# Performance work log

Measured on AMD Instinct MI355X. Metric: run time of the kernel, lower is better.

The kernel has to match this reference:

```python
import jax, jax.numpy as jnp
import numpy as np
from jax import lax

H = 256        # hidden_size
T = 576        # history length (PERIOD*24)
F_T = 24       # future steps
M = 32         # m_features
B = 256        # batch
PERIOD = T // 24
E = 2 * H      # encoder output dim (bidirectional)
EPS = 1e-6     # torch PairwiseDistance eps


def setup_inputs() -> dict:
    key = jax.random.key(0)
    ks = jax.random.split(key, 16)
    rn = lambda k, sh, s=1.0: jax.random.normal(k, sh, jnp.float32) * s
    return {
        "input_encoded": rn(ks[0], (B, T, E)),
        "feature_history1": rn(ks[1], (B, T, M)),
        "y_history": rn(ks[2], (B, T, 1)),               # unused by forward (matches torch)
        "feature_future1": rn(ks[3], (B, F_T, M)),
        "hidden": rn(ks[4], (2, B, H), 0.1),
        "cell": rn(ks[5], (2, B, H), 0.1),
        # attn_layer: Linear(2H+M -> T), Tanh, Linear(T -> T)
        "attn_W1": rn(ks[6], (T, E + M), 0.05), "attn_b1": jnp.zeros((T,), jnp.float32),
        "attn_W2": rn(ks[7], (T, T), 0.05),     "attn_b2": jnp.zeros((T,), jnp.float32),
        # bidirectional 1-layer LSTM, stacked over direction d in {fwd, bwd}
        "W_ih": rn(ks[8], (2, 4 * H, E + M), 0.05),
        "W_hh": rn(ks[9], (2, 4 * H, H), 0.05),
        "b_ih": jnp.zeros((2, 4 * H), jnp.float32),
        "b_hh": jnp.zeros((2, 4 * H), jnp.float32),
        # fc_final: Linear(2H -> H), ReLU, Linear(H -> 1)
        "fcf_W1": rn(ks[10], (H, E), 0.05), "fcf_b1": jnp.zeros((H,), jnp.float32),
        "fcf_W2": rn(ks[11], (1, H), 0.05), "fcf_b2": jnp.zeros((1,), jnp.float32),
    }


def reference(input_encoded, feature_history1, y_history, feature_future1,
              hidden, cell, attn_W1, attn_b1, attn_W2, attn_b2,
              W_ih, W_hh, b_ih, b_hh, fcf_W1, fcf_b1, fcf_W2, fcf_b2):
    b = input_encoded.shape[0]
    # --- period-similarity weights alpha (computed once) ---
    fh = feature_history1.reshape(b, PERIOD, 24, M)                 # [B,period,24,M]
    # pairwise L2 distance between future [B,24,1,M] and history hours [B,24,period,M]
    diff = feature_future1[:, :, None, :] - fh.transpose(0, 2, 1, 3)  # [B,24,period,M]
    dist = jnp.sqrt(jnp.sum((diff + EPS) ** 2, axis=-1))            # [B,24,period]
    dp = 1.0 / jnp.sum(dist, axis=2)                                # rsqrt(.)**2 == 1/x; [B,24]
    alpha = jax.nn.softmax(dp, axis=1)                              # [B,24] (period==24)
    enc = input_encoded.reshape(b, PERIOD, 24, E)                   # [B,period,24,E]
    bias = (b_ih + b_hh)[:, None, :]                                # [2,1,4H]

    def step(carry, ff_t):                                          # ff_t: [B,M]
        h, c = carry                                                # each [2,B,H]
        x = jnp.concatenate([h[0], h[1], ff_t], axis=1)             # [B,2H+M]
        a = jnp.tanh(x @ attn_W1.T + attn_b1) @ attn_W2.T + attn_b2
        a = jax.nn.softmax(a, axis=1)                               # [B,T]
        w = a.reshape(b, PERIOD, 24)                                # [B,period,24]
        # context: sum attention-weighted encodings over each day, then alpha over periods
        ctx = jnp.einsum('bpk,bpke,bp->be', w, enc, alpha)          # [B,E]
        inp = jnp.concatenate([ctx, ff_t], axis=1)                  # [B,2H+M]
        gates = (jnp.einsum('bi,dgi->dbg', inp, W_ih)
                 + jnp.einsum('dbh,dgh->dbg', h, W_hh) + bias)      # [2,B,4H]
        i_g, f_g, g_g, o_g = jnp.split(gates, 4, axis=-1)           # torch gate order i,f,g,o
        c_new = jax.nn.sigmoid(f_g) * c + jax.nn.sigmoid(i_g) * jnp.tanh(g_g)
        h_new = jax.nn.sigmoid(o_g) * jnp.tanh(c_new)               # [2,B,H]
        hh = jnp.concatenate([h_new[0], h_new[1]], axis=1)          # [B,2H]
        y = jax.nn.relu(hh @ fcf_W1.T + fcf_b1) @ fcf_W2.T + fcf_b2  # [B,1]
        return (h_new, c_new), y

    _, ys = lax.scan(step, (hidden, cell), jnp.transpose(feature_future1, (1, 0, 2)))
    return jnp.transpose(ys, (1, 0, 2))                             # [B,f_T,1]
```

## Files before the change

kernel.cpp:

```cpp
#include <hip/hip_runtime.h>
#include <math.h>

#define B_ 256
#define T_ 576
#define FT_ 24
#define M_ 32
#define H_ 256
#define E_ 512
#define KX_ 544
#define G_ 1024
#define ND_ 2048
#define EPS_ 1e-6f

typedef __attribute__((ext_vector_type(8))) short bf8;
typedef __attribute__((ext_vector_type(4))) float f4;

__device__ __forceinline__ float bf2f(unsigned short s) {
    union { unsigned u; float f; } c; c.u = ((unsigned)s) << 16; return c.f;
}
__device__ __forceinline__ short f2bf(float f) {
    union { float f; unsigned u; } c; c.f = f;
    unsigned r = c.u + 0x7fffu + ((c.u >> 16) & 1u);
    return (short)(r >> 16);
}
__device__ __forceinline__ float sigm(float x) { return 1.f / (1.f + expf(-x)); }

__global__ __launch_bounds__(64) void k_alpha(const float* __restrict__ ff,
                                              const float* __restrict__ fhist,
                                              float* __restrict__ alpha) {
    int b = blockIdx.x;
    int t = threadIdx.x;
    float dp = 0.f;
    if (t < 24) {
        float fv[M_];
        const float* fp = ff + (b * FT_ + t) * M_;
        #pragma unroll
        for (int m = 0; m < M_; m++) fv[m] = fp[m];
        float dist = 0.f;
        for (int p = 0; p < 24; p++) {
            const float* hp = fhist + (b * T_ + p * 24 + t) * M_;
            float s = 0.f;
            #pragma unroll
            for (int m = 0; m < M_; m++) { float d = fv[m] - hp[m] + EPS_; s += d * d; }
            dist += sqrtf(s);
        }
        dp = 1.f / dist;
    }
    float v = (t < 24) ? dp : -INFINITY;
    float mx = v;
    for (int off = 32; off; off >>= 1) mx = fmaxf(mx, __shfl_xor(mx, off));
    float e = (t < 24) ? expf(dp - mx) : 0.f;
    float sm = e;
    for (int off = 32; off; off >>= 1) sm += __shfl_xor(sm, off);
    if (t < 24) alpha[b * 24 + t] = e / sm;
}

__global__ __launch_bounds__(256) void k_cast4(const float* __restrict__ src,
                                               short* __restrict__ dst, int n4) {
    int i = blockIdx.x * 256 + threadIdx.x;
    if (i < n4) {
        float4 v = ((const float4*)src)[i];
        short4 o;
        o.x = f2bf(v.x); o.y = f2bf(v.y); o.z = f2bf(v.z); o.w = f2bf(v.w);
        ((short4*)dst)[i] = o;
    }
}

__global__ __launch_bounds__(256) void k_init(const float* __restrict__ hidden,
                                              const float* __restrict__ cell,
                                              const float* __restrict__ ff,
                                              short* __restrict__ x, short* __restrict__ hb,
                                              float* __restrict__ c) {
    int i = blockIdx.x * 256 + threadIdx.x;
    int d = i >> 16, b = (i >> 8) & 255, j = i & 255;
    float h = hidden[i];
    short hv = f2bf(h);
    hb[i] = hv;
    x[b * KX_ + d * H_ + j] = hv;
    c[i] = cell[i];
    if (d == 0 && j < M_) x[b * KX_ + E_ + j] = f2bf(ff[(b * FT_ + 0) * M_ + j]);
}

template <int EPI>
__global__ __launch_bounds__(256) void k_gemm(const short* __restrict__ A, int lda, int K,
                                              const short* __restrict__ W,
                                              const float* __restrict__ bias,
                                              void* __restrict__ out, int ldc) {
    __shared__ short As[64][40];
    __shared__ short Bs[64][40];
    int n0 = blockIdx.x * 64, m0 = blockIdx.y * 64;
    int tid = threadIdx.x, lane = tid & 63, w = tid >> 6;
    int wm = (w & 1) * 32, wn = (w >> 1) * 32;
    int r = tid >> 2, cg = (tid & 3) * 8;
    f4 acc[2][2] = {};
    int nch = K / 32;
    int4 pa = *(const int4*)(A + (m0 + r) * lda + cg);
    int4 pb = *(const int4*)(W + (n0 + r) * K + cg);
    for (int kc = 0; kc < nch; kc++) {
        *(int4*)&As[r][cg] = pa;
        *(int4*)&Bs[r][cg] = pb;
        __syncthreads();
        if (kc + 1 < nch) {
            int ko = (kc + 1) * 32 + cg;
            pa = *(const int4*)(A + (m0 + r) * lda + ko);
            pb = *(const int4*)(W + (n0 + r) * K + ko);
        }
        int fr = lane & 15, fk = (lane >> 4) * 8;
        bf8 a0 = *(const bf8*)&As[wm + fr][fk];
        bf8 a1 = *(const bf8*)&As[wm + 16 + fr][fk];
        bf8 b0 = *(const bf8*)&Bs[wn + fr][fk];
        bf8 b1 = *(const bf8*)&Bs[wn + 16 + fr][fk];
        acc[0][0] = __builtin_amdgcn_mfma_f32_16x16x32_bf16(a0, b0, acc[0][0], 0, 0, 0);
        acc[0][1] = __builtin_amdgcn_mfma_f32_16x16x32_bf16(a0, b1, acc[0][1], 0, 0, 0);
        acc[1][0] = __builtin_amdgcn_mfma_f32_16x16x32_bf16(a1, b0, acc[1][0], 0, 0, 0);
        acc[1][1] = __builtin_amdgcn_mfma_f32_16x16x32_bf16(a1, b1, acc[1][1], 0, 0, 0);
        __syncthreads();
    }
    int colb = n0 + wn + (lane & 15);
    int rowb = m0 + wm + (lane >> 4) * 4;
    #pragma unroll
    for (int im = 0; im < 2; im++)
        #pragma unroll
        for (int in = 0; in < 2; in++) {
            int col = colb + in * 16;
            float bv = bias[col];
            #pragma unroll
            for (int q = 0; q < 4; q++) {
                int row = rowb + im * 16 + q;
                float v = acc[im][in][q] + bv;
                if (EPI == 0)      ((short*)out)[row * ldc + col] = f2bf(tanhf(v));
                else if (EPI == 1) ((float*)out)[row * ldc + col] = v;
                else               ((float*)out)[row * ldc + col] = fmaxf(v, 0.f);
            }
        }
}

template <int BF16E>
__global__ __launch_bounds__(256) void k_ctx(const float* __restrict__ logits,
                                             const float* __restrict__ alpha,
                                             const short* __restrict__ encb,
                                             const float* __restrict__ encf,
                                             float* __restrict__ ctxp) {
    int b = blockIdx.x >> 2, s = blockIdx.x & 3;
    int tid = threadIdx.x;
    __shared__ float wt[T_];
    __shared__ float red[4];
    const float* lg = logits + b * T_;
    float l0 = lg[tid], l1 = lg[tid + 256];
    float l2 = (tid < 64) ? lg[tid + 512] : -INFINITY;
    float mx = fmaxf(fmaxf(l0, l1), l2);
    for (int off = 32; off; off >>= 1) mx = fmaxf(mx, __shfl_xor(mx, off));
    if ((tid & 63) == 0) red[tid >> 6] = mx;
    __syncthreads();
    mx = fmaxf(fmaxf(red[0], red[1]), fmaxf(red[2], red[3]));
    float e0 = expf(l0 - mx), e1 = expf(l1 - mx);
    float e2 = (tid < 64) ? expf(l2 - mx) : 0.f;
    float sm = e0 + e1 + e2;
    for (int off = 32; off; off >>= 1) sm += __shfl_xor(sm, off);
    __syncthreads();
    if ((tid & 63) == 0) red[tid >> 6] = sm;
    __syncthreads();
    float inv = 1.f / (red[0] + red[1] + red[2] + red[3]);
    const float* al = alpha + b * 24;
    wt[tid]       = e0 * inv * al[tid / 24];
    wt[tid + 256] = e1 * inv * al[(tid + 256) / 24];
    if (tid < 64) wt[tid + 512] = e2 * inv * al[(tid + 512) / 24];
    __syncthreads();
    float a0 = 0.f, a1 = 0.f;
    int t0 = s * (T_ / 4);
    if (BF16E) {
        const unsigned* ep = (const unsigned*)(encb + (b * T_ + t0) * E_) + tid;
        for (int t = 0; t < T_ / 4; t++) {
            float wv = wt[t0 + t];
            unsigned u = ep[t * (E_ / 2)];
            a0 += wv * bf2f((unsigned short)(u & 0xffffu));
            a1 += wv * bf2f((unsigned short)(u >> 16));
        }
    } else {
        const float2* ep = (const float2*)(encf + ((size_t)b * T_ + t0) * E_) + tid;
        for (int t = 0; t < T_ / 4; t++) {
            float wv = wt[t0 + t];
            float2 u = ep[t * (E_ / 2)];
            a0 += wv * u.x;
            a1 += wv * u.y;
        }
    }
    float* cp = ctxp + (s * B_ + b) * E_;
    cp[2 * tid] = a0;
    cp[2 * tid + 1] = a1;
}

__global__ __launch_bounds__(256) void k_gates(const float* __restrict__ ctxp,
                                               const float* __restrict__ ff, int step,
                                               const short* __restrict__ hb,
                                               const short* __restrict__ Wih,
                                               const short* __restrict__ Whh,
                                               float* __restrict__ gates) {
    __shared__ short As[64][40];
    __shared__ short Bs[64][40];
    int n0 = blockIdx.x * 64, m0 = blockIdx.y * 64;
    int tid = threadIdx.x, lane = tid & 63, w = tid >> 6;
    int wm = (w & 1) * 32, wn = (w >> 1) * 32;
    int r = tid >> 2, cg = (tid & 3) * 8;
    int b = m0 + r;
    f4 acc[2][2] = {};
    int fr = lane & 15, fk = (lane >> 4) * 8;
    for (int kc = 0; kc < KX_ / 32; kc++) {
        int k = kc * 32 + cg;
        short av[8];
        if (k < E_) {
            const float* c0 = ctxp + b * E_ + k;
            #pragma unroll
            for (int j = 0; j < 8; j++) {
                float v = c0[j] + c0[B_ * E_ + j] + c0[2 * B_ * E_ + j] + c0[3 * B_ * E_ + j];
                av[j] = f2bf(v);
            }
        } else {
            const float* fp = ff + (b * FT_ + step) * M_ + (k - E_);
            #pragma unroll
            for (int j = 0; j < 8; j++) av[j] = f2bf(fp[j]);
        }
        *(int4*)&As[r][cg] = *(int4*)av;
        *(int4*)&Bs[r][cg] = *(const int4*)(Wih + (n0 + r) * KX_ + k);
        __syncthreads();
        bf8 a0 = *(const bf8*)&As[wm + fr][fk];
        bf8 a1 = *(const bf8*)&As[wm + 16 + fr][fk];
        bf8 b0 = *(const bf8*)&Bs[wn + fr][fk];
        bf8 b1 = *(const bf8*)&Bs[wn + 16 + fr][fk];
        acc[0][0] = __builtin_amdgcn_mfma_f32_16x16x32_bf16(a0, b0, acc[0][0], 0, 0, 0);
        acc[0][1] = __builtin_amdgcn_mfma_f32_16x16x32_bf16(a0, b1, acc[0][1], 0, 0, 0);
        acc[1][0] = __builtin_amdgcn_mfma_f32_16x16x32_bf16(a1, b0, acc[1][0], 0, 0, 0);
        acc[1][1] = __builtin_amdgcn_mfma_f32_16x16x32_bf16(a1, b1, acc[1][1], 0, 0, 0);
        __syncthreads();
    }
    int d = n0 >> 10;
    const short* A2 = hb + d * B_ * H_;
    for (int kc = 0; kc < H_ / 32; kc++) {
        int k = kc * 32 + cg;
        *(int4*)&As[r][cg] = *(const int4*)(A2 + b * H_ + k);
        *(int4*)&Bs[r][cg] = *(const int4*)(Whh + (n0 + r) * H_ + k);
        __syncthreads();
        bf8 a0 = *(const bf8*)&As[wm + fr][fk];
        bf8 a1 = *(const bf8*)&As[wm + 16 + fr][fk];
        bf8 b0 = *(const bf8*)&Bs[wn + fr][fk];
        bf8 b1 = *(const bf8*)&Bs[wn + 16 + fr][fk];
        acc[0][0] = __builtin_amdgcn_mfma_f32_16x16x32_bf16(a0, b0, acc[0][0], 0, 0, 0);
        acc[0][1] = __builtin_amdgcn_mfma_f32_16x16x32_bf16(a0, b1, acc[0][1], 0, 0, 0);
        acc[1][0] = __builtin_amdgcn_mfma_f32_16x16x32_bf16(a1, b0, acc[1][0], 0, 0, 0);
        acc[1][1] = __builtin_amdgcn_mfma_f32_16x16x32_bf16(a1, b1, acc[1][1], 0, 0, 0);
        __syncthreads();
    }
    int colb = n0 + wn + (lane & 15);
    int rowb = m0 + wm + (lane >> 4) * 4;
    #pragma unroll
    for (int im = 0; im < 2; im++)
        #pragma unroll
        for (int in = 0; in < 2; in++)
            #pragma unroll
            for (int q = 0; q < 4; q++)
                gates[(rowb + im * 16 + q) * ND_ + colb + in * 16] = acc[im][in][q];
}

__global__ __launch_bounds__(256) void k_lstm(const float* __restrict__ gates,
                                              const float* __restrict__ bih,
                                              const float* __restrict__ bhh,
                                              const float* __restrict__ ff, int step,
                                              float* __restrict__ c, short* __restrict__ hb,
                                              short* __restrict__ x) {
    int i = blockIdx.x * 256 + threadIdx.x;
    int d = i >> 16, b = (i >> 8) & 255, j = i & 255;
    int gb = b * ND_ + d * G_;
    int bb = d * G_;
    float ig = gates[gb + j]       + bih[bb + j]       + bhh[bb + j];
    float fg = gates[gb + 256 + j] + bih[bb + 256 + j] + bhh[bb + 256 + j];
    float gg = gates[gb + 512 + j] + bih[bb + 512 + j] + bhh[bb + 512 + j];
    float og = gates[gb + 768 + j] + bih[bb + 768 + j] + bhh[bb + 768 + j];
    float cv = c[i];
    float cn = sigm(fg) * cv + sigm(ig) * tanhf(gg);
    float hn = sigm(og) * tanhf(cn);
    c[i] = cn;
    short hv = f2bf(hn);
    hb[i] = hv;
    x[b * KX_ + d * H_ + j] = hv;
    if (d == 0 && j < M_ && step + 1 < FT_)
        x[b * KX_ + E_ + j] = f2bf(ff[(b * FT_ + step + 1) * M_ + j]);
}

__global__ __launch_bounds__(256) void k_fc2(const float* __restrict__ z,
                                             const float* __restrict__ w2,
                                             const float* __restrict__ b2,
                                             float* __restrict__ out, int step) {
    int b = blockIdx.x * 4 + (threadIdx.x >> 6);
    int lane = threadIdx.x & 63;
    const float* zr = z + b * H_;
    float s = zr[lane] * w2[lane] + zr[lane + 64] * w2[lane + 64] +
              zr[lane + 128] * w2[lane + 128] + zr[lane + 192] * w2[lane + 192];
    for (int off = 32; off; off >>= 1) s += __shfl_xor(s, off);
    if (lane == 0) out[b * FT_ + step] = s + b2[0];
}

extern "C" void kernel_launch(void* const* d_in, const int* in_sizes, int n_in,
                              void* d_out, int out_size, void* d_ws, size_t ws_size,
                              hipStream_t stream) {
    (void)in_sizes; (void)n_in; (void)out_size;
    const float* enc_f  = (const float*)d_in[0];
    const float* fhist  = (const float*)d_in[1];
    const float* ff     = (const float*)d_in[3];
    const float* hidden = (const float*)d_in[4];
    const float* cell   = (const float*)d_in[5];
    const float* aW1    = (const float*)d_in[6];
    const float* ab1    = (const float*)d_in[7];
    const float* aW2    = (const float*)d_in[8];
    const float* ab2    = (const float*)d_in[9];
    const float* Wih    = (const float*)d_in[10];
    const float* Whh    = (const float*)d_in[11];
    const float* bih    = (const float*)d_in[12];
    const float* bhh    = (const float*)d_in[13];
    const float* fW1    = (const float*)d_in[14];
    const float* fb1    = (const float*)d_in[15];
    const float* fW2    = (const float*)d_in[16];
    const float* fb2    = (const float*)d_in[17];
    float* out = (float*)d_out;

    char* p = (char*)d_ws;
    auto take = [&](size_t n) { char* r = p; p += (n + 255) & ~(size_t)255; return r; };
    float* alpha = (float*)take(B_ * 24 * 4);
    short* xb    = (short*)take(B_ * KX_ * 2);
    short* hb    = (short*)take(2 * B_ * H_ * 2);
    float* cbuf  = (float*)take(2 * B_ * H_ * 4);
    short* s1    = (short*)take(B_ * T_ * 2);
    float* logit = (float*)take(B_ * T_ * 4);
    float* ctxp  = (float*)take(4 * B_ * E_ * 4);
    float* gates = (float*)take(B_ * ND_ * 4);
    float* z     = (float*)take(B_ * H_ * 4);
    short* W1b   = (short*)take(T_ * KX_ * 2);
    short* W2b   = (short*)take(T_ * T_ * 2);
    short* Wihb  = (short*)take(ND_ * KX_ * 2);
    short* Whhb  = (short*)take(ND_ * H_ * 2);
    short* fW1b  = (short*)take(H_ * E_ * 2);
    short* encb  = (short*)take((size_t)B_ * T_ * E_ * 2);
    size_t full_need = (size_t)(p - (char*)d_ws);
    bool use_encb = ws_size >= full_need;

    k_alpha<<<B_, 64, 0, stream>>>(ff, fhist, alpha);
    k_cast4<<<(T_ * KX_ / 4 + 255) / 256, 256, 0, stream>>>(aW1, W1b, T_ * KX_ / 4);
    k_cast4<<<(T_ * T_ / 4 + 255) / 256, 256, 0, stream>>>(aW2, W2b, T_ * T_ / 4);
    k_cast4<<<(ND_ * KX_ / 4 + 255) / 256, 256, 0, stream>>>(Wih, Wihb, ND_ * KX_ / 4);
    k_cast4<<<(ND_ * H_ / 4 + 255) / 256, 256, 0, stream>>>(Whh, Whhb, ND_ * H_ / 4);
    k_cast4<<<(H_ * E_ / 4 + 255) / 256, 256, 0, stream>>>(fW1, fW1b, H_ * E_ / 4);
    if (use_encb)
        k_cast4<<<(B_ * T_ * E_ / 4 + 255) / 256, 256, 0, stream>>>(enc_f, encb, B_ * T_ * E_ / 4);
    k_init<<<(2 * B_ * H_) / 256, 256, 0, stream>>>(hidden, cell, ff, xb, hb, cbuf);

    for (int step = 0; step < FT_; step++) {
        k_gemm<0><<<dim3(T_ / 64, B_ / 64), 256, 0, stream>>>(xb, KX_, KX_, W1b, ab1, s1, T_);
        k_gemm<1><<<dim3(T_ / 64, B_ / 64), 256, 0, stream>>>(s1, T_, T_, W2b, ab2, logit, T_);
        if (use_encb)
            k_ctx<1><<<B_ * 4, 256, 0, stream>>>(logit, alpha, encb, enc_f, ctxp);
        else
            k_ctx<0><<<B_ * 4, 256, 0, stream>>>(logit, alpha, encb, enc_f, ctxp);
        k_gates<<<dim3(ND_ / 64, B_ / 64), 256, 0, stream>>>(ctxp, ff, step, hb, Wihb, Whhb, gates);
        k_lstm<<<(2 * B_ * H_) / 256, 256, 0, stream>>>(gates, bih, bhh, ff, step, cbuf, hb, xb);
        k_gemm<3><<<dim3(H_ / 64, B_ / 64), 256, 0, stream>>>(xb, KX_, E_, fW1b, fb1, z, H_);
        k_fc2<<<B_ / 4, 256, 0, stream>>>(z, fW2, fb2, out, step);
    }
}
```

Before: 2.283 ms.

## Fuse whole decoder loop into one persistent cooperative kernel with grid syncs

```diff
diff --git a/kernel.cpp b/kernel.cpp
--- a/kernel.cpp
+++ b/kernel.cpp
@@ -1,4 +1,5 @@
 #include <hip/hip_runtime.h>
+#include <hip/hip_cooperative_groups.h>
 #include <math.h>
 
 #define B_ 256
@@ -11,6 +12,8 @@
 #define G_ 1024
 #define ND_ 2048
 #define EPS_ 1e-6f
+#define GRID_ 256
+#define NTH_ 65536
 
 typedef __attribute__((ext_vector_type(8))) short bf8;
 typedef __attribute__((ext_vector_type(4))) float f4;
@@ -24,6 +27,300 @@
     return (short)(r >> 16);
 }
 __device__ __forceinline__ float sigm(float x) { return 1.f / (1.f + expf(-x)); }
+
+struct Prm {
+    const float *enc, *fhist, *ff, *hidden, *cell;
+    const float *aW1, *ab1, *aW2, *ab2;
+    const float *Wih, *Whh, *bih, *bhh;
+    const float *fW1, *fb1, *fW2, *fb2;
+    float* out;
+    float *alpha, *cbuf, *logit, *ctx, *gates;
+    short *xb, *s1, *W1b, *W2b, *Wihb, *Whhb, *fW1b, *encb;
+};
+
+struct SMem {
+    union {
+        struct { short As[64][40]; short Bs[64][40]; } g;
+        struct { float wt[T_]; float red[4]; } c;
+    } u;
+    float ypart[64];
+};
+
+__device__ __forceinline__ void gemm64(const short* __restrict__ A, int lda,
+                                       const short* __restrict__ Wt, int ldw, int K,
+                                       short (*As)[40], short (*Bs)[40], int tid,
+                                       f4 acc[2][2]) {
+    int lane = tid & 63, w = tid >> 6;
+    int wm = (w & 1) * 32, wn = (w >> 1) * 32;
+    int r = tid >> 2, cg = (tid & 3) * 8;
+    int fr = lane & 15, fk = (lane >> 4) * 8;
+    int nch = K / 32;
+    int4 pa = *(const int4*)(A + r * lda + cg);
+    int4 pb = *(const int4*)(Wt + r * ldw + cg);
+    for (int kc = 0; kc < nch; kc++) {
+        *(int4*)&As[r][cg] = pa;
+        *(int4*)&Bs[r][cg] = pb;
+        __syncthreads();
+        if (kc + 1 < nch) {
+            int ko = (kc + 1) * 32 + cg;
+            pa = *(const int4*)(A + r * lda + ko);
+            pb = *(const int4*)(Wt + r * ldw + ko);
+        }
+        bf8 a0 = *(const bf8*)&As[wm + fr][fk];
+        bf8 a1 = *(const bf8*)&As[wm + 16 + fr][fk];
+        bf8 b0 = *(const bf8*)&Bs[wn + fr][fk];
+        bf8 b1 = *(const bf8*)&Bs[wn + 16 + fr][fk];
+        acc[0][0] = __builtin_amdgcn_mfma_f32_16x16x32_bf16(a0, b0, acc[0][0], 0, 0, 0);
+        acc[0][1] = __builtin_amdgcn_mfma_f32_16x16x32_bf16(a0, b1, acc[0][1], 0, 0, 0);
+        acc[1][0] = __builtin_amdgcn_mfma_f32_16x16x32_bf16(a1, b0, acc[1][0], 0, 0, 0);
+        acc[1][1] = __builtin_amdgcn_mfma_f32_16x16x32_bf16(a1, b1, acc[1][1], 0, 0, 0);
+        __syncthreads();
+    }
+}
+
+__device__ __forceinline__ void fc_tile(const Prm& p, SMem& sm, int fb, int step, int tid) {
+    int m0 = (fb >> 2) * 64, n0 = (fb & 3) * 64;
+    f4 acc[2][2] = {};
+    gemm64(p.xb + m0 * KX_, KX_, p.fW1b + n0 * E_, E_, E_, sm.u.g.As, sm.u.g.Bs, tid, acc);
+    if (tid < 64) sm.ypart[tid] = 0.f;
+    __syncthreads();
+    int lane = tid & 63, w = tid >> 6;
+    int wm = (w & 1) * 32, wn = (w >> 1) * 32;
+    int colb = n0 + wn + (lane & 15);
+    int rloc = wm + (lane >> 4) * 4;
+    #pragma unroll
+    for (int im = 0; im < 2; im++)
+        #pragma unroll
+        for (int q = 0; q < 4; q++) {
+            float s = 0.f;
+            #pragma unroll
+            for (int in = 0; in < 2; in++) {
+                int col = colb + in * 16;
+                s += fmaxf(acc[im][in][q] + p.fb1[col], 0.f) * p.fW2[col];
+            }
+            #pragma unroll
+            for (int off = 1; off < 16; off <<= 1) s += __shfl_xor(s, off);
+            if ((lane & 15) == 0) atomicAdd(&sm.ypart[rloc + im * 16 + q], s);
+        }
+    __syncthreads();
+    if (tid < 64) atomicAdd(&p.out[(m0 + tid) * FT_ + step], sm.ypart[tid]);
+}
+
+__global__ __launch_bounds__(256) void k_all(Prm p) {
+    cooperative_groups::grid_group grid = cooperative_groups::this_grid();
+    __shared__ SMem sm;
+    const int blk = blockIdx.x, tid = threadIdx.x;
+
+    {
+        int gt = blk * 256 + tid;
+        auto cast = [&](const float* s, short* d, int n4) {
+            for (int i = gt; i < n4; i += NTH_) {
+                float4 v = ((const float4*)s)[i];
+                short4 o; o.x = f2bf(v.x); o.y = f2bf(v.y); o.z = f2bf(v.z); o.w = f2bf(v.w);
+                ((short4*)d)[i] = o;
+            }
+        };
+        cast(p.aW1, p.W1b, T_ * KX_ / 4);
+        cast(p.aW2, p.W2b, T_ * T_ / 4);
+        cast(p.Wih, p.Wihb, ND_ * KX_ / 4);
+        cast(p.Whh, p.Whhb, ND_ * H_ / 4);
+        cast(p.fW1, p.fW1b, H_ * E_ / 4);
+        cast(p.enc, p.encb, B_ * T_ * E_ / 4);
+        for (int idx = gt; idx < B_ * 24; idx += NTH_) {
+            int b = idx / 24, tt = idx % 24;
+            const float* fp = p.ff + (b * FT_ + tt) * M_;
+            float fv[M_];
+            #pragma unroll
+            for (int m = 0; m < M_; m++) fv[m] = fp[m];
+            float dist = 0.f;
+            for (int pp = 0; pp < 24; pp++) {
+                const float* hp = p.fhist + (b * T_ + pp * 24 + tt) * M_;
+                float s = 0.f;
+                #pragma unroll
+                for (int m = 0; m < M_; m++) { float d = fv[m] - hp[m] + EPS_; s += d * d; }
+                dist += sqrtf(s);
+            }
+            p.alpha[idx] = 1.f / dist;
+        }
+        for (int i = gt; i < 2 * B_ * H_; i += NTH_) {
+            int d = i >> 16, b = (i >> 8) & 255, j = i & 255;
+            p.xb[b * KX_ + d * H_ + j] = f2bf(p.hidden[i]);
+            p.cbuf[i] = p.cell[i];
+            if (d == 0 && j < M_) p.xb[b * KX_ + E_ + j] = f2bf(p.ff[(b * FT_ + 0) * M_ + j]);
+        }
+    }
+    grid.sync();
+
+    for (int t = 0; t < FT_; t++) {
+        if (blk < 36) {
+            int n0 = (blk % 9) * 64, m0 = (blk / 9) * 64;
+            f4 acc[2][2] = {};
+            gemm64(p.xb + m0 * KX_, KX_, p.W1b + n0 * KX_, KX_, KX_,
+                   sm.u.g.As, sm.u.g.Bs, tid, acc);
+            int lane = tid & 63, w = tid >> 6;
+            int wm = (w & 1) * 32, wn = (w >> 1) * 32;
+            int colb = n0 + wn + (lane & 15);
+            int rowb = m0 + wm + (lane >> 4) * 4;
+            #pragma unroll
+            for (int im = 0; im < 2; im++)
+                #pragma unroll
+                for (int in = 0; in < 2; in++) {
+                    int col = colb + in * 16;
+                    float bv = p.ab1[col];
+                    #pragma unroll
+                    for (int q = 0; q < 4; q++)
+                        p.s1[(rowb + im * 16 + q) * T_ + col] = f2bf(tanhf(acc[im][in][q] + bv));
+                }
+        } else if (t == 0) {
+            if (blk == 36) {
+                int b = tid;
+                float v[24], mx = -INFINITY;
+                #pragma unroll
+                for (int k = 0; k < 24; k++) { v[k] = p.alpha[b * 24 + k]; mx = fmaxf(mx, v[k]); }
+                float s = 0.f;
+                #pragma unroll
+                for (int k = 0; k < 24; k++) { v[k] = expf(v[k] - mx); s += v[k]; }
+                float inv = 1.f / s;
+                #pragma unroll
+                for (int k = 0; k < 24; k++) p.alpha[b * 24 + k] = v[k] * inv;
+            }
+        } else if (blk < 52) {
+            fc_tile(p, sm, blk - 36, t - 1, tid);
+        }
+        grid.sync();
+
+        if (blk < 36) {
+            int n0 = (blk % 9) * 64, m0 = (blk / 9) * 64;
+            f4 acc[2][2] = {};
+            gemm64(p.s1 + m0 * T_, T_, p.W2b + n0 * T_, T_, T_,
+                   sm.u.g.As, sm.u.g.Bs, tid, acc);
+            int lane = tid & 63, w = tid >> 6;
+            int wm = (w & 1) * 32, wn = (w >> 1) * 32;
+            int colb = n0 + wn + (lane & 15);
+            int rowb = m0 + wm + (lane >> 4) * 4;
+            #pragma unroll
+            for (int im = 0; im < 2; im++)
+                #pragma unroll
+                for (int in = 0; in < 2; in++) {
+                    int col = colb + in * 16;
+                    float bv = p.ab2[col];
+                    #pragma unroll
+                    for (int q = 0; q < 4; q++)
+                        p.logit[(rowb + im * 16 + q) * T_ + col] = acc[im][in][q] + bv;
+                }
+        }
+        grid.sync();
+
+        {
+            int b = blk;
+            const float* lg = p.logit + b * T_;
+            float l0 = lg[tid], l1 = lg[tid + 256];
+            float l2 = (tid < 64) ? lg[tid + 512] : -INFINITY;
+            float mx = fmaxf(fmaxf(l0, l1), l2);
+            for (int off = 32; off; off >>= 1) mx = fmaxf(mx, __shfl_xor(mx, off));
+            if ((tid & 63) == 0) sm.u.c.red[tid >> 6] = mx;
+            __syncthreads();
+            mx = fmaxf(fmaxf(sm.u.c.red[0], sm.u.c.red[1]),
+                       fmaxf(sm.u.c.red[2], sm.u.c.red[3]));
+            float e0 = expf(l0 - mx), e1 = expf(l1 - mx);
+            float e2 = (tid < 64) ? expf(l2 - mx) : 0.f;
+            float s = e0 + e1 + e2;
+            for (int off = 32; off; off >>= 1) s += __shfl_xor(s, off);
+            __syncthreads();
+            if ((tid & 63) == 0) sm.u.c.red[tid >> 6] = s;
+            __syncthreads();
+            float inv = 1.f / (sm.u.c.red[0] + sm.u.c.red[1] + sm.u.c.red[2] + sm.u.c.red[3]);
+            const float* al = p.alpha + b * 24;
+            sm.u.c.wt[tid]       = e0 * inv * al[tid / 24];
+            sm.u.c.wt[tid + 256] = e1 * inv * al[(tid + 256) / 24];
+            if (tid < 64) sm.u.c.wt[tid + 512] = e2 * inv * al[(tid + 512) / 24];
+            __syncthreads();
+            float a0 = 0.f, a1 = 0.f;
+            const unsigned* ep = (const unsigned*)(p.encb + (size_t)b * T_ * E_) + tid;
+            #pragma unroll 8
+            for (int tt = 0; tt < T_; tt++) {
+                float wv = sm.u.c.wt[tt];
+                unsigned u = ep[(size_t)tt * (E_ / 2)];
+                a0 += wv * bf2f((unsigned short)(u & 0xffffu));
+                a1 += wv * bf2f((unsigned short)(u >> 16));
+            }
+            p.ctx[b * E_ + 2 * tid]     = a0;
+            p.ctx[b * E_ + 2 * tid + 1] = a1;
+        }
+        grid.sync();
+
+        if (blk < 128) {
+            int n0 = (blk & 31) * 64, m0 = (blk >> 5) * 64;
+            int lane = tid & 63, w = tid >> 6;
+            int wm = (w & 1) * 32, wn = (w >> 1) * 32;
+            int r = tid >> 2, cg = (tid & 3) * 8;
+            int fr = lane & 15, fk = (lane >> 4) * 8;
+            f4 acc[2][2] = {};
+            for (int kc = 0; kc < KX_ / 32; kc++) {
+                int k = kc * 32 + cg;
+                union { short s[8]; int4 v; } av;
+                if (k < E_) {
+                    const float* c0 = p.ctx + (m0 + r) * E_ + k;
+                    #pragma unroll
+                    for (int j = 0; j < 8; j++) av.s[j] = f2bf(c0[j]);
+                } else {
+                    const float* fp = p.ff + ((m0 + r) * FT_ + t) * M_ + (k - E_);
+                    #pragma unroll
+                    for (int j = 0; j < 8; j++) av.s[j] = f2bf(fp[j]);
+                }
+                *(int4*)&sm.u.g.As[r][cg] = av.v;
+                *(int4*)&sm.u.g.Bs[r][cg] = *(const int4*)(p.Wihb + (n0 + r) * KX_ + k);
+                __syncthreads();
+                bf8 a0 = *(const bf8*)&sm.u.g.As[wm + fr][fk];
+                bf8 a1 = *(const bf8*)&sm.u.g.As[wm + 16 + fr][fk];
+                bf8 b0 = *(const bf8*)&sm.u.g.Bs[wn + fr][fk];
+                bf8 b1 = *(const bf8*)&sm.u.g.Bs[wn + 16 + fr][fk];
+                acc[0][0] = __builtin_amdgcn_mfma_f32_16x16x32_bf16(a0, b0, acc[0][0], 0, 0, 0);
+                acc[0][1] = __builtin_amdgcn_mfma_f32_16x16x32_bf16(a0, b1, acc[0][1], 0, 0, 0);
+                acc[1][0] = __builtin_amdgcn_mfma_f32_16x16x32_bf16(a1, b0, acc[1][0], 0, 0, 0);
+                acc[1][1] = __builtin_amdgcn_mfma_f32_16x16x32_bf16(a1, b1, acc[1][1], 0, 0, 0);
+                __syncthreads();
+            }
+            int d = n0 >> 10;
+            gemm64(p.xb + m0 * KX_ + d * H_, KX_, p.Whhb + n0 * H_, H_, H_,
+                   sm.u.g.As, sm.u.g.Bs, tid, acc);
+            int colb = n0 + wn + (lane & 15);
+            int rowb = m0 + wm + (lane >> 4) * 4;
+            #pragma unroll
+            for (int im = 0; im < 2; im++)
+                #pragma unroll
+                for (int in = 0; in < 2; in++)
+                    #pragma unroll
+                    for (int q = 0; q < 4; q++)
+                        p.gates[(rowb + im * 16 + q) * ND_ + colb + in * 16] = acc[im][in][q];
+        }
+        grid.sync();
+
+        #pragma unroll
+        for (int half = 0; half < 2; half++) {
+            int i = blk * 512 + half * 256 + tid;
+            int d = i >> 16, b = (i >> 8) & 255, j = i & 255;
+            int gb = b * ND_ + d * G_, bb = d * G_;
+            float ig = p.gates[gb + j]       + p.bih[bb + j]       + p.bhh[bb + j];
+            float fg = p.gates[gb + 256 + j] + p.bih[bb + 256 + j] + p.bhh[bb + 256 + j];
+            float gg = p.gates[gb + 512 + j] + p.bih[bb + 512 + j] + p.bhh[bb + 512 + j];
+            float og = p.gates[gb + 768 + j] + p.bih[bb + 768 + j] + p.bhh[bb + 768 + j];
+            float cv = p.cbuf[i];
+            float cn = sigm(fg) * cv + sigm(ig) * tanhf(gg);
+            float hn = sigm(og) * tanhf(cn);
+            p.cbuf[i] = cn;
+            p.xb[b * KX_ + d * H_ + j] = f2bf(hn);
+            if (d == 0) {
+                if (j < M_ && t + 1 < FT_)
+                    p.xb[b * KX_ + E_ + j] = f2bf(p.ff[(b * FT_ + t + 1) * M_ + j]);
+                if (j == 0) p.out[b * FT_ + t] = p.fb2[0];
+            }
+        }
+        grid.sync();
+    }
+
+    if (blk < 16) fc_tile(p, sm, blk, FT_ - 1, tid);
+}
 
 __global__ __launch_bounds__(64) void k_alpha(const float* __restrict__ ff,
                                               const float* __restrict__ fhist,
@@ -37,8 +334,8 @@
         #pragma unroll
         for (int m = 0; m < M_; m++) fv[m] = fp[m];
         float dist = 0.f;
-        for (int p = 0; p < 24; p++) {
-            const float* hp = fhist + (b * T_ + p * 24 + t) * M_;
+        for (int pp = 0; pp < 24; pp++) {
+            const float* hp = fhist + (b * T_ + pp * 24 + t) * M_;
             float s = 0.f;
             #pragma unroll
             for (int m = 0; m < M_; m++) { float d = fv[m] - hp[m] + EPS_; s += d * d; }
@@ -50,9 +347,9 @@
     float mx = v;
     for (int off = 32; off; off >>= 1) mx = fmaxf(mx, __shfl_xor(mx, off));
     float e = (t < 24) ? expf(dp - mx) : 0.f;
-    float sm = e;
-    for (int off = 32; off; off >>= 1) sm += __shfl_xor(sm, off);
-    if (t < 24) alpha[b * 24 + t] = e / sm;
+    float sme = e;
+    for (int off = 32; off; off >>= 1) sme += __shfl_xor(sme, off);
+    if (t < 24) alpha[b * 24 + t] = e / sme;
 }
 
 __global__ __launch_bounds__(256) void k_cast4(const float* __restrict__ src,
@@ -69,14 +366,10 @@
 __global__ __launch_bounds__(256) void k_init(const float* __restrict__ hidden,
                                               const float* __restrict__ cell,
                                               const float* __restrict__ ff,
-                                              short* __restrict__ x, short* __restrict__ hb,
-                                              float* __restrict__ c) {
+                                              short* __restrict__ x, float* __restrict__ c) {
     int i = blockIdx.x * 256 + threadIdx.x;
     int d = i >> 16, b = (i >> 8) & 255, j = i & 255;
-    float h = hidden[i];
-    short hv = f2bf(h);
-    hb[i] = hv;
-    x[b * KX_ + d * H_ + j] = hv;
+    x[b * KX_ + d * H_ + j] = f2bf(hidden[i]);
     c[i] = cell[i];
     if (d == 0 && j < M_) x[b * KX_ + E_ + j] = f2bf(ff[(b * FT_ + 0) * M_ + j]);
 }
@@ -89,33 +382,11 @@
     __shared__ short As[64][40];
     __shared__ short Bs[64][40];
     int n0 = blockIdx.x * 64, m0 = blockIdx.y * 64;
-    int tid = threadIdx.x, lane = tid & 63, w = tid >> 6;
+    int tid = threadIdx.x;
+    f4 acc[2][2] = {};
+    gemm64(A + m0 * lda, lda, W + n0 * K, K, K, As, Bs, tid, acc);
+    int lane = tid & 63, w = tid >> 6;
     int wm = (w & 1) * 32, wn = (w >> 1) * 32;
-    int r = tid >> 2, cg = (tid & 3) * 8;
-    f4 acc[2][2] = {};
-    int nch = K / 32;
-    int4 pa = *(const int4*)(A + (m0 + r) * lda + cg);
-    int4 pb = *(const int4*)(W + (n0 + r) * K + cg);
-    for (int kc = 0; kc < nch; kc++) {
-        *(int4*)&As[r][cg] = pa;
-        *(int4*)&Bs[r][cg] = pb;
-        __syncthreads();
-        if (kc + 1 < nch) {
-            int ko = (kc + 1) * 32 + cg;
-            pa = *(const int4*)(A + (m0 + r) * lda + ko);
-            pb = *(const int4*)(W + (n0 + r) * K + ko);
-        }
-        int fr = lane & 15, fk = (lane >> 4) * 8;
-        bf8 a0 = *(const bf8*)&As[wm + fr][fk];
-        bf8 a1 = *(const bf8*)&As[wm + 16 + fr][fk];
-        bf8 b0 = *(const bf8*)&Bs[wn + fr][fk];
-        bf8 b1 = *(const bf8*)&Bs[wn + 16 + fr][fk];
-        acc[0][0] = __builtin_amdgcn_mfma_f32_16x16x32_bf16(a0, b0, acc[0][0], 0, 0, 0);
-        acc[0][1] = __builtin_amdgcn_mfma_f32_16x16x32_bf16(a0, b1, acc[0][1], 0, 0, 0);
-        acc[1][0] = __builtin_amdgcn_mfma_f32_16x16x32_bf16(a1, b0, acc[1][0], 0, 0, 0);
-        acc[1][1] = __builtin_amdgcn_mfma_f32_16x16x32_bf16(a1, b1, acc[1][1], 0, 0, 0);
-        __syncthreads();
-    }
     int colb = n0 + wn + (lane & 15);
     int rowb = m0 + wm + (lane >> 4) * 4;
     #pragma unroll
@@ -128,18 +399,15 @@
             for (int q = 0; q < 4; q++) {
                 int row = rowb + im * 16 + q;
                 float v = acc[im][in][q] + bv;
-                if (EPI == 0)      ((short*)out)[row * ldc + col] = f2bf(tanhf(v));
-                else if (EPI == 1) ((float*)out)[row * ldc + col] = v;
-                else               ((float*)out)[row * ldc + col] = fmaxf(v, 0.f);
-            }
-        }
-}
-
-template <int BF16E>
+                if (EPI == 0) ((short*)out)[row * ldc + col] = f2bf(tanhf(v));
+                else          ((float*)out)[row * ldc + col] = v;
+            }
+        }
+}
+
 __global__ __launch_bounds__(256) void k_ctx(const float* __restrict__ logits,
                                              const float* __restrict__ alpha,
                                              const short* __restrict__ encb,
-                                             const float* __restrict__ encf,
                                              float* __restrict__ ctxp) {
     int b = blockIdx.x >> 2, s = blockIdx.x & 3;
     int tid = threadIdx.x;
@@ -155,10 +423,10 @@
     mx = fmaxf(fmaxf(red[0], red[1]), fmaxf(red[2], red[3]));
     float e0 = expf(l0 - mx), e1 = expf(l1 - mx);
     float e2 = (tid < 64) ? expf(l2 - mx) : 0.f;
-    float sm = e0 + e1 + e2;
-    for (int off = 32; off; off >>= 1) sm += __shfl_xor(sm, off);
-    __syncthreads();
-    if ((tid & 63) == 0) red[tid >> 6] = sm;
+    float sme = e0 + e1 + e2;
+    for (int off = 32; off; off >>= 1) sme += __shfl_xor(sme, off);
+    __syncthreads();
+    if ((tid & 63) == 0) red[tid >> 6] = sme;
     __syncthreads();
     float inv = 1.f / (red[0] + red[1] + red[2] + red[3]);
     const float* al = alpha + b * 24;
@@ -168,22 +436,12 @@
     __syncthreads();
     float a0 = 0.f, a1 = 0.f;
     int t0 = s * (T_ / 4);
-    if (BF16E) {
-        const unsigned* ep = (const unsigned*)(encb + (b * T_ + t0) * E_) + tid;
-        for (int t = 0; t < T_ / 4; t++) {
-            float wv = wt[t0 + t];
-            unsigned u = ep[t * (E_ / 2)];
-            a0 += wv * bf2f((unsigned short)(u & 0xffffu));
-            a1 += wv * bf2f((unsigned short)(u >> 16));
-        }
-    } else {
-        const float2* ep = (const float2*)(encf + ((size_t)b * T_ + t0) * E_) + tid;
-        for (int t = 0; t < T_ / 4; t++) {
-            float wv = wt[t0 + t];
-            float2 u = ep[t * (E_ / 2)];
-            a0 += wv * u.x;
-            a1 += wv * u.y;
-        }
+    const unsigned* ep = (const unsigned*)(encb + ((size_t)b * T_ + t0) * E_) + tid;
+    for (int t = 0; t < T_ / 4; t++) {
+        float wv = wt[t0 + t];
+        unsigned u = ep[(size_t)t * (E_ / 2)];
+        a0 += wv * bf2f((unsigned short)(u & 0xffffu));
+        a1 += wv * bf2f((unsigned short)(u >> 16));
     }
     float* cp = ctxp + (s * B_ + b) * E_;
     cp[2 * tid] = a0;
@@ -192,7 +450,7 @@
 
 __global__ __launch_bounds__(256) void k_gates(const float* __restrict__ ctxp,
                                                const float* __restrict__ ff, int step,
-                                               const short* __restrict__ hb,
+                                               const short* __restrict__ xb,
                                                const short* __restrict__ Wih,
                                                const short* __restrict__ Whh,
                                                float* __restrict__ gates) {
@@ -207,20 +465,20 @@
     int fr = lane & 15, fk = (lane >> 4) * 8;
     for (int kc = 0; kc < KX_ / 32; kc++) {
         int k = kc * 32 + cg;
-        short av[8];
+        union { short s[8]; int4 v; } av;
         if (k < E_) {
             const float* c0 = ctxp + b * E_ + k;
             #pragma unroll
             for (int j = 0; j < 8; j++) {
                 float v = c0[j] + c0[B_ * E_ + j] + c0[2 * B_ * E_ + j] + c0[3 * B_ * E_ + j];
-                av[j] = f2bf(v);
+                av.s[j] = f2bf(v);
             }
         } else {
             const float* fp = ff + (b * FT_ + step) * M_ + (k - E_);
             #pragma unroll
-            for (int j = 0; j < 8; j++) av[j] = f2bf(fp[j]);
-        }
-        *(int4*)&As[r][cg] = *(int4*)av;
+            for (int j = 0; j < 8; j++) av.s[j] = f2bf(fp[j]);
+        }
+        *(int4*)&As[r][cg] = av.v;
         *(int4*)&Bs[r][cg] = *(const int4*)(Wih + (n0 + r) * KX_ + k);
         __syncthreads();
         bf8 a0 = *(const bf8*)&As[wm + fr][fk];
@@ -234,22 +492,7 @@
         __syncthreads();
     }
     int d = n0 >> 10;
-    const short* A2 = hb + d * B_ * H_;
-    for (int kc = 0; kc < H_ / 32; kc++) {
-        int k = kc * 32 + cg;
-        *(int4*)&As[r][cg] = *(const int4*)(A2 + b * H_ + k);
-        *(int4*)&Bs[r][cg] = *(const int4*)(Whh + (n0 + r) * H_ + k);
-        __syncthreads();
-        bf8 a0 = *(const bf8*)&As[wm + fr][fk];
-        bf8 a1 = *(const bf8*)&As[wm + 16 + fr][fk];
-        bf8 b0 = *(const bf8*)&Bs[wn + fr][fk];
-        bf8 b1 = *(const bf8*)&Bs[wn + 16 + fr][fk];
-        acc[0][0] = __builtin_amdgcn_mfma_f32_16x16x32_bf16(a0, b0, acc[0][0], 0, 0, 0);
-        acc[0][1] = __builtin_amdgcn_mfma_f32_16x16x32_bf16(a0, b1, acc[0][1], 0, 0, 0);
-        acc[1][0] = __builtin_amdgcn_mfma_f32_16x16x32_bf16(a1, b0, acc[1][0], 0, 0, 0);
-        acc[1][1] = __builtin_amdgcn_mfma_f32_16x16x32_bf16(a1, b1, acc[1][1], 0, 0, 0);
-        __syncthreads();
-    }
+    gemm64(xb + m0 * KX_ + d * H_, KX_, Whh + n0 * H_, H_, H_, As, Bs, tid, acc);
     int colb = n0 + wn + (lane & 15);
     int rowb = m0 + wm + (lane >> 4) * 4;
     #pragma unroll
@@ -265,8 +508,9 @@
                                               const float* __restrict__ bih,
                                               const float* __restrict__ bhh,
                                               const float* __restrict__ ff, int step,
-                                              float* __restrict__ c, short* __restrict__ hb,
-                                              short* __restrict__ x) {
+                                              float* __restrict__ c, short* __restrict__ x,
+                                              const float* __restrict__ fb2,
+                                              float* __restrict__ out) {
     int i = blockIdx.x * 256 + threadIdx.x;
     int d = i >> 16, b = (i >> 8) & 255, j = i & 255;
     int gb = b * ND_ + d * G_;
@@ -279,30 +523,54 @@
     float cn = sigm(fg) * cv + sigm(ig) * tanhf(gg);
     float hn = sigm(og) * tanhf(cn);
     c[i] = cn;
-    short hv = f2bf(hn);
-    hb[i] = hv;
-    x[b * KX_ + d * H_ + j] = hv;
-    if (d == 0 && j < M_ && step + 1 < FT_)
-        x[b * KX_ + E_ + j] = f2bf(ff[(b * FT_ + step + 1) * M_ + j]);
-}
-
-__global__ __launch_bounds__(256) void k_fc2(const float* __restrict__ z,
-                                             const float* __restrict__ w2,
-                                             const float* __restrict__ b2,
-                                             float* __restrict__ out, int step) {
-    int b = blockIdx.x * 4 + (threadIdx.x >> 6);
-    int lane = threadIdx.x & 63;
-    const float* zr = z + b * H_;
-    float s = zr[lane] * w2[lane] + zr[lane + 64] * w2[lane + 64] +
-              zr[lane + 128] * w2[lane + 128] + zr[lane + 192] * w2[lane + 192];
-    for (int off = 32; off; off >>= 1) s += __shfl_xor(s, off);
-    if (lane == 0) out[b * FT_ + step] = s + b2[0];
+    x[b * KX_ + d * H_ + j] = f2bf(hn);
+    if (d == 0) {
+        if (j < M_ && step + 1 < FT_)
+            x[b * KX_ + E_ + j] = f2bf(ff[(b * FT_ + step + 1) * M_ + j]);
+        if (j == 0) out[b * FT_ + step] = fb2[0];
+    }
+}
+
+__global__ __launch_bounds__(256) void k_fc(const short* __restrict__ xb,
+                                            const short* __restrict__ fW1b,
+                                            const float* __restrict__ fb1,
+                                            const float* __restrict__ fW2,
+                                            float* __restrict__ out, int step) {
+    __shared__ short As[64][40];
+    __shared__ short Bs[64][40];
+    __shared__ float ypart[64];
+    int fb = blockIdx.x, tid = threadIdx.x;
+    int m0 = (fb >> 2) * 64, n0 = (fb & 3) * 64;
+    f4 acc[2][2] = {};
+    gemm64(xb + m0 * KX_, KX_, fW1b + n0 * E_, E_, E_, As, Bs, tid, acc);
+    if (tid < 64) ypart[tid] = 0.f;
+    __syncthreads();
+    int lane = tid & 63, w = tid >> 6;
+    int wm = (w & 1) * 32, wn = (w >> 1) * 32;
+    int colb = n0 + wn + (lane & 15);
+    int rloc = wm + (lane >> 4) * 4;
+    #pragma unroll
+    for (int im = 0; im < 2; im++)
+        #pragma unroll
+        for (int q = 0; q < 4; q++) {
+            float s = 0.f;
+            #pragma unroll
+            for (int in = 0; in < 2; in++) {
+                int col = colb + in * 16;
+                s += fmaxf(acc[im][in][q] + fb1[col], 0.f) * fW2[col];
+            }
+            #pragma unroll
+            for (int off = 1; off < 16; off <<= 1) s += __shfl_xor(s, off);
+            if ((lane & 15) == 0) atomicAdd(&ypart[rloc + im * 16 + q], s);
+        }
+    __syncthreads();
+    if (tid < 64) atomicAdd(&out[(m0 + tid) * FT_ + step], ypart[tid]);
 }
 
 extern "C" void kernel_launch(void* const* d_in, const int* in_sizes, int n_in,
                               void* d_out, int out_size, void* d_ws, size_t ws_size,
                               hipStream_t stream) {
-    (void)in_sizes; (void)n_in; (void)out_size;
+    (void)in_sizes; (void)n_in; (void)out_size; (void)ws_size;
     const float* enc_f  = (const float*)d_in[0];
     const float* fhist  = (const float*)d_in[1];
     const float* ff     = (const float*)d_in[3];
@@ -322,25 +590,36 @@
     const float* fb2    = (const float*)d_in[17];
     float* out = (float*)d_out;
 
-    char* p = (char*)d_ws;
-    auto take = [&](size_t n) { char* r = p; p += (n + 255) & ~(size_t)255; return r; };
+    char* pws = (char*)d_ws;
+    auto take = [&](size_t n) { char* r = pws; pws += (n + 255) & ~(size_t)255; return r; };
     float* alpha = (float*)take(B_ * 24 * 4);
     short* xb    = (short*)take(B_ * KX_ * 2);
-    short* hb    = (short*)take(2 * B_ * H_ * 2);
     float* cbuf  = (float*)take(2 * B_ * H_ * 4);
     short* s1    = (short*)take(B_ * T_ * 2);
     float* logit = (float*)take(B_ * T_ * 4);
     float* ctxp  = (float*)take(4 * B_ * E_ * 4);
     float* gates = (float*)take(B_ * ND_ * 4);
-    float* z     = (float*)take(B_ * H_ * 4);
     short* W1b   = (short*)take(T_ * KX_ * 2);
     short* W2b   = (short*)take(T_ * T_ * 2);
     short* Wihb  = (short*)take(ND_ * KX_ * 2);
     short* Whhb  = (short*)take(ND_ * H_ * 2);
     short* fW1b  = (short*)take(H_ * E_ * 2);
     short* encb  = (short*)take((size_t)B_ * T_ * E_ * 2);
-    size_t full_need = (size_t)(p - (char*)d_ws);
-    bool use_encb = ws_size >= full_need;
+
+    Prm prm;
+    prm.enc = enc_f; prm.fhist = fhist; prm.ff = ff; prm.hidden = hidden; prm.cell = cell;
+    prm.aW1 = aW1; prm.ab1 = ab1; prm.aW2 = aW2; prm.ab2 = ab2;
+    prm.Wih = Wih; prm.Whh = Whh; prm.bih = bih; prm.bhh = bhh;
+    prm.fW1 = fW1; prm.fb1 = fb1; prm.fW2 = fW2; prm.fb2 = fb2;
+    prm.out = out;
+    prm.alpha = alpha; prm.cbuf = cbuf; prm.logit = logit; prm.ctx = ctxp; prm.gates = gates;
+    prm.xb = xb; prm.s1 = s1; prm.W1b = W1b; prm.W2b = W2b;
+    prm.Wihb = Wihb; prm.Whhb = Whhb; prm.fW1b = fW1b; prm.encb = encb;
+
+    void* kargs[] = { (void*)&prm };
+    hipError_t rc = hipLaunchCooperativeKernel((const void*)k_all, dim3(GRID_), dim3(256),
+                                               kargs, 0, stream);
+    if (rc == hipSuccess) return;
 
     k_alpha<<<B_, 64, 0, stream>>>(ff, fhist, alpha);
     k_cast4<<<(T_ * KX_ / 4 + 255) / 256, 256, 0, stream>>>(aW1, W1b, T_ * KX_ / 4);
@@ -348,20 +627,14 @@
     k_cast4<<<(ND_ * KX_ / 4 + 255) / 256, 256, 0, stream>>>(Wih, Wihb, ND_ * KX_ / 4);
     k_cast4<<<(ND_ * H_ / 4 + 255) / 256, 256, 0, stream>>>(Whh, Whhb, ND_ * H_ / 4);
     k_cast4<<<(H_ * E_ / 4 + 255) / 256, 256, 0, stream>>>(fW1, fW1b, H_ * E_ / 4);
-    if (use_encb)
-        k_cast4<<<(B_ * T_ * E_ / 4 + 255) / 256, 256, 0, stream>>>(enc_f, encb, B_ * T_ * E_ / 4);
-    k_init<<<(2 * B_ * H_) / 256, 256, 0, stream>>>(hidden, cell, ff, xb, hb, cbuf);
-
+    k_cast4<<<(B_ * T_ * E_ / 4 + 255) / 256, 256, 0, stream>>>(enc_f, encb, B_ * T_ * E_ / 4);
+    k_init<<<(2 * B_ * H_) / 256, 256, 0, stream>>>(hidden, cell, ff, xb, cbuf);
     for (int step = 0; step < FT_; step++) {
         k_gemm<0><<<dim3(T_ / 64, B_ / 64), 256, 0, stream>>>(xb, KX_, KX_, W1b, ab1, s1, T_);
         k_gemm<1><<<dim3(T_ / 64, B_ / 64), 256, 0, stream>>>(s1, T_, T_, W2b, ab2, logit, T_);
-        if (use_encb)
-            k_ctx<1><<<B_ * 4, 256, 0, stream>>>(logit, alpha, encb, enc_f, ctxp);
-        else
-            k_ctx<0><<<B_ * 4, 256, 0, stream>>>(logit, alpha, encb, enc_f, ctxp);
-        k_gates<<<dim3(ND_ / 64, B_ / 64), 256, 0, stream>>>(ctxp, ff, step, hb, Wihb, Whhb, gates);
-        k_lstm<<<(2 * B_ * H_) / 256, 256, 0, stream>>>(gates, bih, bhh, ff, step, cbuf, hb, xb);
-        k_gemm<3><<<dim3(H_ / 64, B_ / 64), 256, 0, stream>>>(xb, KX_, E_, fW1b, fb1, z, H_);
-        k_fc2<<<B_ / 4, 256, 0, stream>>>(z, fW2, fb2, out, step);
-    }
-}
+        k_ctx<<<B_ * 4, 256, 0, stream>>>(logit, alpha, encb, ctxp);
+        k_gates<<<dim3(ND_ / 64, B_ / 64), 256, 0, stream>>>(ctxp, ff, step, xb, Wihb, Whhb, gates);
+        k_lstm<<<(2 * B_ * H_) / 256, 256, 0, stream>>>(gates, bih, bhh, ff, step, cbuf, xb, fb2, out);
+        k_fc<<<16, 256, 0, stream>>>(xb, fW1b, fb1, fW2, out, step);
+    }
+}
```

Result: slower. 5.525 ms (+142.0%).
